# Performance work log

Hardware: AMD Instinct MI355X
Metric: run time of the kernel (lower is better)

Reference implementation:

```python
import jax, jax.numpy as jnp
import numpy as np

B, T, C, H, E, K = 4, 2048, 512, 2048, 8, 2


def setup_inputs() -> dict:
    key = jax.random.key(0)
    ks = jax.random.split(key, 7)
    s_r = 1.0 / np.sqrt(C)
    s_h = 1.0 / np.sqrt(H)
    return {
        "x": jax.random.normal(ks[0], (B, T, C), dtype=jnp.float32),
        "Wr": jax.random.uniform(ks[1], (C, E), jnp.float32, -s_r, s_r),
        "br": jax.random.uniform(ks[2], (E,), jnp.float32, -s_r, s_r),
        "W1": jax.random.uniform(ks[3], (E, C, H), jnp.float32, -s_r, s_r),
        "b1": jax.random.uniform(ks[4], (E, H), jnp.float32, -s_r, s_r),
        "W2": jax.random.uniform(ks[5], (E, H, C), jnp.float32, -s_h, s_h),
        "b2": jax.random.uniform(ks[6], (E, C), jnp.float32, -s_h, s_h),
    }


def reference(x, Wr, br, W1, b1, W2, b2):
    # Router logits [B,T,E]
    logits = jnp.einsum("btc,ce->bte", x, Wr) + br
    topk_vals, topk_idx = jax.lax.top_k(logits, K)  # [B,T,K]
    scores = jax.nn.softmax(topk_vals, axis=-1)  # softmax over the K selected
    # Combine weights per expert: gate[b,t,e] = sum_k scores[b,t,k]*(idx==e)
    onehot = jax.nn.one_hot(topk_idx, E, dtype=x.dtype)  # [B,T,K,E]
    gate = jnp.einsum("btk,btke->bte", scores, onehot)  # [B,T,E]
    # Dense-masked expert MLPs (tokens not routed to e have gate==0)
    h = jax.nn.relu(jnp.einsum("btc,ech->bteh", x, W1) + b1)  # [B,T,E,H]
    y = jnp.einsum("bteh,ehc->btec", h, W2) + b2  # [B,T,E,C]
    out = jnp.einsum("btec,bte->btc", y, gate)  # weighted combine
    return logits, topk_idx, out
```

## Files before the change

### kernel.cpp

```cpp
#include <hip/hip_runtime.h>
#include <hip/hip_bf16.h>

#define NTOK 8192
#define NASN 16384
#define C_ 512
#define H_ 2048
#define E_ 8
#define RBC 2048

typedef __bf16 bf16x8 __attribute__((ext_vector_type(8)));
typedef float f32x4 __attribute__((ext_vector_type(4)));

#define WS_COUNTS 0
#define WS_OFFS   65536
#define WS_T1S    65792
#define WS_INFO   66048
#define WS_TOKL   (WS_INFO + NTOK*16)
#define WS_SLOTS  (WS_TOKL + NASN*4)
#define WS_XBF    (WS_SLOTS + NTOK*8)
#define WS_W1B    (WS_XBF + (size_t)NTOK*C_*2)
#define WS_W2B    (WS_W1B + (size_t)E_*H_*C_*2)
#define WS_HS     (WS_W2B + (size_t)E_*H_*C_*2)
#define WS_YS     WS_XBF

__device__ __forceinline__ unsigned int f2bf(float f) {
  __hip_bfloat16 h = __float2bfloat16(f);
  return (unsigned int)*(unsigned short*)&h;
}
__device__ __forceinline__ float bf2f(unsigned int u) {
  return __int_as_float((u & 0xffffu) << 16);
}

__device__ __forceinline__ void g2l16(const unsigned short* g, unsigned short* l) {
  __builtin_amdgcn_global_load_lds(
      (const __attribute__((address_space(1))) unsigned int*)g,
      (__attribute__((address_space(3))) unsigned int*)l, 16, 0, 0);
}

__device__ __forceinline__ void stage_decode(int L, int& brow, int& q) {
  int s = L >> 3, slot = L & 7;
  int v = slot ^ (s & 7);
  brow = 2*s + (v >> 2);
  q = v & 3;
}

__global__ __launch_bounds__(256) void k_fused(
    const float* __restrict__ x, const float* __restrict__ Wr,
    const float* __restrict__ br, float* __restrict__ out_logits,
    float* __restrict__ out_idx, int4* __restrict__ info,
    int* __restrict__ counts, unsigned short* __restrict__ Xbf,
    const float* __restrict__ W1, unsigned short* __restrict__ W1b,
    const float* __restrict__ W2, unsigned short* __restrict__ W2b)
{
  __shared__ float tileS[128][33];
  __shared__ int bc[8];
  int b = blockIdx.x;
  int tid = threadIdx.x;

  if (b < RBC) {
    if (tid < 8) bc[tid] = 0;
    __syncthreads();
    int t = b * 4 + (tid >> 6);
    int lane = tid & 63;
    const float4* xr = (const float4*)(x + (size_t)t * C_);
    float4 x0 = xr[lane*2], x1 = xr[lane*2+1];
    uint4 pk;
    pk.x = f2bf(x0.x) | (f2bf(x0.y) << 16);
    pk.y = f2bf(x0.z) | (f2bf(x0.w) << 16);
    pk.z = f2bf(x1.x) | (f2bf(x1.y) << 16);
    pk.w = f2bf(x1.z) | (f2bf(x1.w) << 16);
    *(uint4*)(Xbf + (size_t)t * C_ + lane*8) = pk;

    float xs[8] = {x0.x,x0.y,x0.z,x0.w,x1.x,x1.y,x1.z,x1.w};
    float acc[8] = {0,0,0,0,0,0,0,0};
    #pragma unroll
    for (int j = 0; j < 8; j++) {
      const float4* w = (const float4*)(Wr + (size_t)(lane*8+j) * E_);
      float4 w0 = w[0], w1 = w[1];
      float we[8] = {w0.x,w0.y,w0.z,w0.w,w1.x,w1.y,w1.z,w1.w};
      #pragma unroll
      for (int e = 0; e < 8; e++) acc[e] += xs[j] * we[e];
    }
    #pragma unroll
    for (int off = 1; off < 64; off <<= 1) {
      #pragma unroll
      for (int e = 0; e < 8; e++) acc[e] += __shfl_xor(acc[e], off, 64);
    }
    #pragma unroll
    for (int e = 0; e < 8; e++) acc[e] += br[e];
    if (lane == 0) {
      #pragma unroll
      for (int e = 0; e < 8; e++) out_logits[t*8 + e] = acc[e];
      int i0 = 0; float v0 = acc[0];
      #pragma unroll
      for (int e = 1; e < 8; e++) if (acc[e] > v0) { v0 = acc[e]; i0 = e; }
      int i1 = -1; float v1 = -1e30f;
      #pragma unroll
      for (int e = 0; e < 8; e++) if (e != i0 && acc[e] > v1) { v1 = acc[e]; i1 = e; }
      float d = expf(v1 - v0);
      float s1 = d / (1.0f + d);
      float s0 = 1.0f - s1;
      out_idx[t*2]     = (float)i0;
      out_idx[t*2 + 1] = (float)i1;
      info[t] = make_int4(i0, i1, __float_as_int(s0), __float_as_int(s1));
      atomicAdd(&bc[i0], 1);
      atomicAdd(&bc[i1], 1);
    }
    __syncthreads();
    if (tid < 8) counts[b*8 + tid] = bc[tid];
    return;
  }

  const float* in; unsigned short* outp; int R, S, bx, by, bz;
  if (b < 2*RBC) {
    int bb = b - RBC;
    in = W1; outp = W1b; R = C_; S = H_;
    bx = bb & 63; by = (bb >> 6) & 3; bz = bb >> 8;
  } else {
    int bb = b - 2*RBC;
    in = W2; outp = W2b; R = H_; S = C_;
    bx = bb & 15; by = (bb >> 4) & 15; bz = bb >> 8;
  }
  size_t zo = (size_t)bz * R * S;
  in += zo; outp += zo;
  int r0 = by * 128, s0 = bx * 32;
  #pragma unroll
  for (int i = 0; i < 16; i++) {
    int lin = i*256 + tid;
    int rr = lin >> 5, ss = lin & 31;
    tileS[rr][ss] = in[(size_t)(r0 + rr) * S + s0 + ss];
  }
  __syncthreads();
  #pragma unroll
  for (int i = 0; i < 4; i++) {
    int lin = i*256 + tid;
    int ss = lin >> 5, rq = lin & 31;
    ushort4 v;
    v.x = (unsigned short)f2bf(tileS[rq*4+0][ss]);
    v.y = (unsigned short)f2bf(tileS[rq*4+1][ss]);
    v.z = (unsigned short)f2bf(tileS[rq*4+2][ss]);
    v.w = (unsigned short)f2bf(tileS[rq*4+3][ss]);
    *(ushort4*)(outp + (size_t)(s0 + ss) * R + r0 + rq*4) = v;
  }
}

__global__ __launch_bounds__(64) void k_prefscatter(
    const int* __restrict__ counts, const int4* __restrict__ info,
    int* __restrict__ tokl, int2* __restrict__ slots2,
    int* __restrict__ offs, int* __restrict__ t1s)
{
  __shared__ int full_s[8][8];
  __shared__ int part_s[8][8];
  __shared__ int tot_s[8];
  __shared__ int off_s[9];
  __shared__ int cur[8];
  int c = blockIdx.x, t = threadIdx.x;
  int e = t & 7, g = t >> 3;
  int lim = c * 16;
  int full = 0, part = 0;
  for (int i = 0; i < 256; i++) {
    int rb = g*256 + i;
    int v = counts[rb*8 + e];
    full += v;
    if (rb < lim) part += v;
  }
  full_s[e][g] = full; part_s[e][g] = part;
  __syncthreads();
  if (t < 8) {
    int s = 0;
    #pragma unroll
    for (int gg = 0; gg < 8; gg++) s += full_s[t][gg];
    tot_s[t] = s;
  }
  __syncthreads();
  if (t == 0) {
    int o = 0;
    off_s[0] = 0;
    for (int ee = 0; ee < 8; ee++) { o += tot_s[ee]; off_s[ee+1] = o; }
    if (c == 0) {
      offs[0] = 0; t1s[0] = 0;
      int tt = 0;
      for (int ee = 0; ee < 8; ee++) {
        offs[ee+1] = off_s[ee+1];
        tt += (tot_s[ee] + 127) >> 7;
        t1s[ee+1] = tt;
      }
    }
  }
  __syncthreads();
  if (t < 8) {
    int mg = c >> 4;
    int bse = off_s[t];
    #pragma unroll
    for (int gg = 0; gg < 8; gg++) if (gg < mg) bse += full_s[t][gg];
    bse += part_s[t][mg];
    cur[t] = bse;
  }
  __syncthreads();
  int tok = c*64 + t;
  int4 nfo = info[tok];
  int r0 = atomicAdd(&cur[nfo.x], 1);
  int r1 = atomicAdd(&cur[nfo.y], 1);
  tokl[r0] = tok;
  tokl[r1] = tok;
  slots2[tok] = make_int2(r0, r1);
}

#define KLOOP(KI)                                                              \
  {                                                                            \
    int cOff = 0, sOff = 2*8192;                                               \
    for (int ki = 0; ki < (KI); ki++) {                                        \
      if (ki + 1 < (KI))                                                       \
        asm volatile("s_waitcnt vmcnt(2)" ::: "memory");                       \
      else                                                                     \
        asm volatile("s_waitcnt vmcnt(0)" ::: "memory");                       \
      asm volatile("s_barrier" ::: "memory");                                  \
      if (ki + 2 < (KI)) {                                                     \
        int off_ = (ki + 2) * 32;                                              \
        unsigned short* nb_ = AB + sOff;                                       \
        g2l16(ga + off_, nb_ + lao);                                           \
        g2l16(gb + off_, nb_ + lbo);                                           \
      }                                                                        \
      const unsigned short* Ap_ = AB + cOff;                                   \
      const unsigned short* Bp_ = Ap_ + 4096;                                  \
      bf16x8 af0 = *(const bf16x8*)&Ap_[wm*32 + 0*512 + rbase];                \
      bf16x8 af1 = *(const bf16x8*)&Ap_[wm*32 + 1*512 + rbase];                \
      bf16x8 bf0 = *(const bf16x8*)&Bp_[wn*32 + 0*512 + rbase];                \
      bf16x8 bf1 = *(const bf16x8*)&Bp_[wn*32 + 1*512 + rbase];                \
      __builtin_amdgcn_s_setprio(1);                                           \
      acc[0][0] = __builtin_amdgcn_mfma_f32_16x16x32_bf16(af0, bf0, acc[0][0], 0, 0, 0); \
      acc[0][1] = __builtin_amdgcn_mfma_f32_16x16x32_bf16(af0, bf1, acc[0][1], 0, 0, 0); \
      acc[1][0] = __builtin_amdgcn_mfma_f32_16x16x32_bf16(af1, bf0, acc[1][0], 0, 0, 0); \
      acc[1][1] = __builtin_amdgcn_mfma_f32_16x16x32_bf16(af1, bf1, acc[1][1], 0, 0, 0); \
      __builtin_amdgcn_s_setprio(0);                                           \
      bf16x8 af2 = *(const bf16x8*)&Ap_[wm*32 + 2*512 + rbase];                \
      bf16x8 af3 = *(const bf16x8*)&Ap_[wm*32 + 3*512 + rbase];                \
      __builtin_amdgcn_s_setprio(1);                                           \
      acc[2][0] = __builtin_amdgcn_mfma_f32_16x16x32_bf16(af2, bf0, acc[2][0], 0, 0, 0); \
      acc[2][1] = __builtin_amdgcn_mfma_f32_16x16x32_bf16(af2, bf1, acc[2][1], 0, 0, 0); \
      acc[3][0] = __builtin_amdgcn_mfma_f32_16x16x32_bf16(af3, bf0, acc[3][0], 0, 0, 0); \
      acc[3][1] = __builtin_amdgcn_mfma_f32_16x16x32_bf16(af3, bf1, acc[3][1], 0, 0, 0); \
      __builtin_amdgcn_s_setprio(0);                                           \
      asm volatile("s_waitcnt lgkmcnt(0)" ::: "memory");                       \
      cOff += 8192; if (cOff == 3*8192) cOff = 0;                              \
      sOff += 8192; if (sOff == 3*8192) sOff = 0;                              \
    }                                                                          \
  }

__global__ __launch_bounds__(512) void k_gemm1(
    const unsigned short* __restrict__ Xbf, const int* __restrict__ tokl,
    const unsigned short* __restrict__ W1b,
    const float* __restrict__ b1, unsigned short* __restrict__ Hs,
    const int* __restrict__ offs, const int* __restrict__ t1s)
{
  __shared__ __align__(16) unsigned short AB[3*8192];
  int b = blockIdx.x;
  int mo = b >> 7, rr = b & 127;
  int n0 = (rr >> 3) * 128;
  int mt = mo*8 + (rr & 7);
  if (mt >= t1s[8]) return;
  int e = 0;
  #pragma unroll
  for (int i = 0; i < 7; i++) if (mt >= t1s[e+1]) e++;
  int row0 = offs[e] + (mt - t1s[e]) * 128;
  int rowEnd = offs[e+1];
  int tid = threadIdx.x, lane = tid & 63, w = tid >> 6;
  int wm = (w >> 2) * 64, wn = (w & 3) * 32;
  int quad = lane >> 4, l16 = lane & 15;
  const f32x4 zero = {0.f, 0.f, 0.f, 0.f};
  f32x4 acc[4][2];
  #pragma unroll
  for (int i = 0; i < 4; i++)
    #pragma unroll
    for (int j = 0; j < 2; j++) acc[i][j] = zero;
  const unsigned short* Bsrc = W1b + ((size_t)e * H_ + n0) * C_;

  const unsigned short* ga; const unsigned short* gb;
  int lao, lbo;
  {
    int L = w*64 + lane;
    int brow, q; stage_decode(L, brow, q);
    int gr = row0 + brow; gr = gr < NASN-1 ? gr : NASN-1;
    int trow = tokl[gr];
    ga = Xbf + (size_t)trow * C_ + q*8;
    gb = Bsrc + (size_t)brow * C_ + q*8;
    lao = w*512;
    lbo = 4096 + w*512;
  }
  int rbase = (l16>>1)*64 + ((((l16&1)<<2) + quad) ^ (l16>>1))*8;
  const int KI = C_ / 32;

  g2l16(ga, AB + lao);            g2l16(gb, AB + lbo);
  g2l16(ga + 32, AB + 8192 + lao); g2l16(gb + 32, AB + 8192 + lbo);

  KLOOP(KI);

  unsigned short* Lt = AB + w*2048;
  #pragma unroll
  for (int j = 0; j < 2; j++) {
    int n = n0 + wn + j*16 + l16;
    float bias = b1[e * H_ + n];
    #pragma unroll
    for (int i = 0; i < 4; i++)
      #pragma unroll
      for (int r = 0; r < 4; r++) {
        float v = acc[i][j][r] + bias;
        Lt[(i*16 + quad*4 + r)*32 + j*16 + l16] = (unsigned short)f2bf(v > 0.f ? v : 0.f);
      }
  }
  #pragma unroll
  for (int it = 0; it < 4; it++) {
    int rloc = it*16 + (lane >> 2);
    int m = row0 + wm + rloc;
    uint4 vv = *(uint4*)&Lt[rloc*32 + (lane & 3)*8];
    if (m < rowEnd)
      *(uint4*)(Hs + (size_t)m * H_ + n0 + wn + (lane & 3)*8) = vv;
  }
}

__global__ __launch_bounds__(512) void k_gemm2(
    const unsigned short* __restrict__ Hs, const unsigned short* __restrict__ W2b,
    const float* __restrict__ b2, unsigned short* __restrict__ Ys,
    const int* __restrict__ offs, const int* __restrict__ t1s)
{
  __shared__ __align__(16) unsigned short AB[3*8192];
  int b = blockIdx.x;
  int mo = b >> 5, rr = b & 31;
  int n0 = (rr >> 3) * 128;
  int mt = mo*8 + (rr & 7);
  if (mt >= t1s[8]) return;
  int e = 0;
  #pragma unroll
  for (int i = 0; i < 7; i++) if (mt >= t1s[e+1]) e++;
  int row0 = offs[e] + (mt - t1s[e]) * 128;
  int rowEnd = offs[e+1];
  int tid = threadIdx.x, lane = tid & 63, w = tid >> 6;
  int wm = (w >> 2) * 64, wn = (w & 3) * 32;
  int quad = lane >> 4, l16 = lane & 15;
  const f32x4 zero = {0.f, 0.f, 0.f, 0.f};
  f32x4 acc[4][2];
  #pragma unroll
  for (int i = 0; i < 4; i++)
    #pragma unroll
    for (int j = 0; j < 2; j++) acc[i][j] = zero;
  const unsigned short* Bsrc = W2b + ((size_t)e * C_ + n0) * H_;

  const unsigned short* ga; const unsigned short* gb;
  int lao, lbo;
  {
    int L = w*64 + lane;
    int brow, q; stage_decode(L, brow, q);
    int gr = row0 + brow; gr = gr < NASN-1 ? gr : NASN-1;
    ga = Hs + (size_t)gr * H_ + q*8;
    gb = Bsrc + (size_t)brow * H_ + q*8;
    lao = w*512;
    lbo = 4096 + w*512;
  }
  int rbase = (l16>>1)*64 + ((((l16&1)<<2) + quad) ^ (l16>>1))*8;
  const int KI = H_ / 32;

  g2l16(ga, AB + lao);            g2l16(gb, AB + lbo);
  g2l16(ga + 32, AB + 8192 + lao); g2l16(gb + 32, AB + 8192 + lbo);

  KLOOP(KI);

  unsigned short* Lt = AB + w*2048;
  #pragma unroll
  for (int j = 0; j < 2; j++) {
    int n = n0 + wn + j*16 + l16;
    float bias = b2[e * C_ + n];
    #pragma unroll
    for (int i = 0; i < 4; i++)
      #pragma unroll
      for (int r = 0; r < 4; r++)
        Lt[(i*16 + quad*4 + r)*32 + j*16 + l16] =
            (unsigned short)f2bf(acc[i][j][r] + bias);
  }
  #pragma unroll
  for (int it = 0; it < 4; it++) {
    int rloc = it*16 + (lane >> 2);
    int m = row0 + wm + rloc;
    uint4 vv = *(uint4*)&Lt[rloc*32 + (lane & 3)*8];
    if (m < rowEnd)
      *(uint4*)(Ys + (size_t)m * C_ + n0 + wn + (lane & 3)*8) = vv;
  }
}

__global__ __launch_bounds__(256) void k_combine(
    const unsigned short* __restrict__ Ys, const int4* __restrict__ info,
    const int2* __restrict__ slots2, float* __restrict__ outp)
{
  int t = blockIdx.x * 4 + (threadIdx.x >> 6);
  int lane = threadIdx.x & 63;
  int4 nfo = info[t];
  int2 ss = slots2[t];
  float g0 = __int_as_float(nfo.z), g1 = __int_as_float(nfo.w);
  uint4 a = *(const uint4*)(Ys + (size_t)ss.x * C_ + lane*8);
  uint4 bb = *(const uint4*)(Ys + (size_t)ss.y * C_ + lane*8);
  unsigned int au[4] = {a.x, a.y, a.z, a.w};
  unsigned int bu[4] = {bb.x, bb.y, bb.z, bb.w};
  float vals[8];
  #pragma unroll
  for (int q = 0; q < 4; q++) {
    vals[q*2]   = g0*bf2f(au[q])       + g1*bf2f(bu[q]);
    vals[q*2+1] = g0*bf2f(au[q] >> 16) + g1*bf2f(bu[q] >> 16);
  }
  float4 o0, o1;
  o0.x = vals[0]; o0.y = vals[1]; o0.z = vals[2]; o0.w = vals[3];
  o1.x = vals[4]; o1.y = vals[5]; o1.z = vals[6]; o1.w = vals[7];
  float4* o = (float4*)(outp + (size_t)t * C_ + lane*8);
  o[0] = o0;
  o[1] = o1;
}

extern "C" void kernel_launch(void* const* d_in, const int* in_sizes, int n_in,
                              void* d_out, int out_size, void* d_ws, size_t ws_size,
                              hipStream_t stream)
{
  const float* x  = (const float*)d_in[0];
  const float* Wr = (const float*)d_in[1];
  const float* br = (const float*)d_in[2];
  const float* W1 = (const float*)d_in[3];
  const float* b1 = (const float*)d_in[4];
  const float* W2 = (const float*)d_in[5];
  const float* b2 = (const float*)d_in[6];
  float* out = (float*)d_out;
  char* ws = (char*)d_ws;

  int*  counts = (int*)(ws + WS_COUNTS);
  int*  offs   = (int*)(ws + WS_OFFS);
  int*  t1s    = (int*)(ws + WS_T1S);
  int4* info   = (int4*)(ws + WS_INFO);
  int*  tokl   = (int*)(ws + WS_TOKL);
  int2* slots2 = (int2*)(ws + WS_SLOTS);
  unsigned short* Xbf = (unsigned short*)(ws + WS_XBF);
  unsigned short* W1b = (unsigned short*)(ws + WS_W1B);
  unsigned short* W2b = (unsigned short*)(ws + WS_W2B);
  unsigned short* Hs  = (unsigned short*)(ws + WS_HS);
  unsigned short* Ys  = (unsigned short*)(ws + WS_YS);

  k_fused<<<3*RBC, 256, 0, stream>>>(x, Wr, br, out, out + 65536, info,
                                     counts, Xbf, W1, W1b, W2, W2b);
  k_prefscatter<<<128, 64, 0, stream>>>(counts, info, tokl, slots2, offs, t1s);
  k_gemm1<<<17*128, 512, 0, stream>>>(Xbf, tokl, W1b, b1, Hs, offs, t1s);
  k_gemm2<<<17*32, 512, 0, stream>>>(Hs, W2b, b2, Ys, offs, t1s);
  k_combine<<<NTOK/4, 256, 0, stream>>>(Ys, info, slots2, out + 81920);
}
```

Measured before the change: 266.8 us.

## Use 2 warps per 128x128 GEMM tile with 64x128 per-warp subtiles

Both expert GEMM kernels now launch 128 threads (2 waves) per 128x128 output tile instead of 512 (8 waves). Each wave computes a 64x128 subtile with 32 MFMA accumulators, reusing each A fragment across 8 B fragments. Each thread issues 4x more global-to-LDS copies, and the vmcnt wait is raised to match. This cuts LDS fragment reads per MFMA, at the cost of far more accumulator registers, lower occupancy and fewer waves to hide latency.

```diff
diff --git a/kernel.cpp b/kernel.cpp
--- a/kernel.cpp
+++ b/kernel.cpp
@@ -211,35 +211,35 @@
     int cOff = 0, sOff = 2*8192;                                               \
     for (int ki = 0; ki < (KI); ki++) {                                        \
       if (ki + 1 < (KI))                                                       \
-        asm volatile("s_waitcnt vmcnt(2)" ::: "memory");                       \
+        asm volatile("s_waitcnt vmcnt(8)" ::: "memory");                       \
       else                                                                     \
         asm volatile("s_waitcnt vmcnt(0)" ::: "memory");                       \
       asm volatile("s_barrier" ::: "memory");                                  \
       if (ki + 2 < (KI)) {                                                     \
         int off_ = (ki + 2) * 32;                                              \
         unsigned short* nb_ = AB + sOff;                                       \
-        g2l16(ga + off_, nb_ + lao);                                           \
-        g2l16(gb + off_, nb_ + lbo);                                           \
+        _Pragma("unroll")                                                      \
+        for (int j = 0; j < 4; j++) {                                          \
+          g2l16(ga[j] + off_, nb_ + lao[j]);                                   \
+          g2l16(gb[j] + off_, nb_ + lbo[j]);                                   \
+        }                                                                      \
       }                                                                        \
       const unsigned short* Ap_ = AB + cOff;                                   \
       const unsigned short* Bp_ = Ap_ + 4096;                                  \
-      bf16x8 af0 = *(const bf16x8*)&Ap_[wm*32 + 0*512 + rbase];                \
-      bf16x8 af1 = *(const bf16x8*)&Ap_[wm*32 + 1*512 + rbase];                \
-      bf16x8 bf0 = *(const bf16x8*)&Bp_[wn*32 + 0*512 + rbase];                \
-      bf16x8 bf1 = *(const bf16x8*)&Bp_[wn*32 + 1*512 + rbase];                \
+      bf16x8 af_[4], bf_[8];                                                   \
+      _Pragma("unroll")                                                        \
+      for (int i = 0; i < 4; i++)                                              \
+        af_[i] = *(const bf16x8*)&Ap_[wmul + i*512 + rbase];                   \
+      _Pragma("unroll")                                                        \
+      for (int j = 0; j < 8; j++)                                              \
+        bf_[j] = *(const bf16x8*)&Bp_[j*512 + rbase];                          \
       __builtin_amdgcn_s_setprio(1);                                           \
-      acc[0][0] = __builtin_amdgcn_mfma_f32_16x16x32_bf16(af0, bf0, acc[0][0], 0, 0, 0); \
-      acc[0][1] = __builtin_amdgcn_mfma_f32_16x16x32_bf16(af0, bf1, acc[0][1], 0, 0, 0); \
-      acc[1][0] = __builtin_amdgcn_mfma_f32_16x16x32_bf16(af1, bf0, acc[1][0], 0, 0, 0); \
-      acc[1][1] = __builtin_amdgcn_mfma_f32_16x16x32_bf16(af1, bf1, acc[1][1], 0, 0, 0); \
-      __builtin_amdgcn_s_setprio(0);                                           \
-      bf16x8 af2 = *(const bf16x8*)&Ap_[wm*32 + 2*512 + rbase];                \
-      bf16x8 af3 = *(const bf16x8*)&Ap_[wm*32 + 3*512 + rbase];                \
-      __builtin_amdgcn_s_setprio(1);                                           \
-      acc[2][0] = __builtin_amdgcn_mfma_f32_16x16x32_bf16(af2, bf0, acc[2][0], 0, 0, 0); \
-      acc[2][1] = __builtin_amdgcn_mfma_f32_16x16x32_bf16(af2, bf1, acc[2][1], 0, 0, 0); \
-      acc[3][0] = __builtin_amdgcn_mfma_f32_16x16x32_bf16(af3, bf0, acc[3][0], 0, 0, 0); \
-      acc[3][1] = __builtin_amdgcn_mfma_f32_16x16x32_bf16(af3, bf1, acc[3][1], 0, 0, 0); \
+      _Pragma("unroll")                                                        \
+      for (int i = 0; i < 4; i++)                                              \
+        _Pragma("unroll")                                                      \
+        for (int j = 0; j < 8; j++)                                            \
+          acc[i][j] = __builtin_amdgcn_mfma_f32_16x16x32_bf16(                 \
+              af_[i], bf_[j], acc[i][j], 0, 0, 0);                             \
       __builtin_amdgcn_s_setprio(0);                                           \
       asm volatile("s_waitcnt lgkmcnt(0)" ::: "memory");                       \
       cOff += 8192; if (cOff == 3*8192) cOff = 0;                              \
@@ -247,7 +247,7 @@
     }                                                                          \
   }
 
-__global__ __launch_bounds__(512) void k_gemm1(
+__global__ __launch_bounds__(128) void k_gemm1(
     const unsigned short* __restrict__ Xbf, const int* __restrict__ tokl,
     const unsigned short* __restrict__ W1b,
     const float* __restrict__ b1, unsigned short* __restrict__ Hs,
@@ -265,60 +265,63 @@
   int row0 = offs[e] + (mt - t1s[e]) * 128;
   int rowEnd = offs[e+1];
   int tid = threadIdx.x, lane = tid & 63, w = tid >> 6;
-  int wm = (w >> 2) * 64, wn = (w & 3) * 32;
+  int wmul = w * 2048;
   int quad = lane >> 4, l16 = lane & 15;
   const f32x4 zero = {0.f, 0.f, 0.f, 0.f};
-  f32x4 acc[4][2];
+  f32x4 acc[4][8];
   #pragma unroll
   for (int i = 0; i < 4; i++)
     #pragma unroll
-    for (int j = 0; j < 2; j++) acc[i][j] = zero;
+    for (int j = 0; j < 8; j++) acc[i][j] = zero;
   const unsigned short* Bsrc = W1b + ((size_t)e * H_ + n0) * C_;
 
-  const unsigned short* ga; const unsigned short* gb;
-  int lao, lbo;
-  {
-    int L = w*64 + lane;
+  const unsigned short* ga[4]; const unsigned short* gb[4];
+  int lao[4], lbo[4];
+  #pragma unroll
+  for (int j = 0; j < 4; j++) {
+    int L = (w*4 + j)*64 + lane;
     int brow, q; stage_decode(L, brow, q);
     int gr = row0 + brow; gr = gr < NASN-1 ? gr : NASN-1;
     int trow = tokl[gr];
-    ga = Xbf + (size_t)trow * C_ + q*8;
-    gb = Bsrc + (size_t)brow * C_ + q*8;
-    lao = w*512;
-    lbo = 4096 + w*512;
+    ga[j] = Xbf + (size_t)trow * C_ + q*8;
+    gb[j] = Bsrc + (size_t)brow * C_ + q*8;
+    lao[j] = (w*4 + j)*512;
+    lbo[j] = 4096 + (w*4 + j)*512;
   }
   int rbase = (l16>>1)*64 + ((((l16&1)<<2) + quad) ^ (l16>>1))*8;
   const int KI = C_ / 32;
 
-  g2l16(ga, AB + lao);            g2l16(gb, AB + lbo);
-  g2l16(ga + 32, AB + 8192 + lao); g2l16(gb + 32, AB + 8192 + lbo);
+  #pragma unroll
+  for (int j = 0; j < 4; j++) { g2l16(ga[j], AB + lao[j]); g2l16(gb[j], AB + lbo[j]); }
+  #pragma unroll
+  for (int j = 0; j < 4; j++) { g2l16(ga[j] + 32, AB + 8192 + lao[j]); g2l16(gb[j] + 32, AB + 8192 + lbo[j]); }
 
   KLOOP(KI);
 
-  unsigned short* Lt = AB + w*2048;
-  #pragma unroll
-  for (int j = 0; j < 2; j++) {
-    int n = n0 + wn + j*16 + l16;
+  unsigned short* Lt = AB + w*8192;
+  #pragma unroll
+  for (int j = 0; j < 8; j++) {
+    int n = n0 + j*16 + l16;
     float bias = b1[e * H_ + n];
     #pragma unroll
     for (int i = 0; i < 4; i++)
       #pragma unroll
       for (int r = 0; r < 4; r++) {
         float v = acc[i][j][r] + bias;
-        Lt[(i*16 + quad*4 + r)*32 + j*16 + l16] = (unsigned short)f2bf(v > 0.f ? v : 0.f);
+        Lt[(i*16 + quad*4 + r)*128 + j*16 + l16] = (unsigned short)f2bf(v > 0.f ? v : 0.f);
       }
   }
   #pragma unroll
-  for (int it = 0; it < 4; it++) {
-    int rloc = it*16 + (lane >> 2);
-    int m = row0 + wm + rloc;
-    uint4 vv = *(uint4*)&Lt[rloc*32 + (lane & 3)*8];
+  for (int it = 0; it < 16; it++) {
+    int rloc = it*4 + (lane >> 4);
+    int m = row0 + w*64 + rloc;
+    uint4 vv = *(uint4*)&Lt[rloc*128 + (lane & 15)*8];
     if (m < rowEnd)
-      *(uint4*)(Hs + (size_t)m * H_ + n0 + wn + (lane & 3)*8) = vv;
-  }
-}
-
-__global__ __launch_bounds__(512) void k_gemm2(
+      *(uint4*)(Hs + (size_t)m * H_ + n0 + (lane & 15)*8) = vv;
+  }
+}
+
+__global__ __launch_bounds__(128) void k_gemm2(
     const unsigned short* __restrict__ Hs, const unsigned short* __restrict__ W2b,
     const float* __restrict__ b2, unsigned short* __restrict__ Ys,
     const int* __restrict__ offs, const int* __restrict__ t1s)
@@ -335,54 +338,57 @@
   int row0 = offs[e] + (mt - t1s[e]) * 128;
   int rowEnd = offs[e+1];
   int tid = threadIdx.x, lane = tid & 63, w = tid >> 6;
-  int wm = (w >> 2) * 64, wn = (w & 3) * 32;
+  int wmul = w * 2048;
   int quad = lane >> 4, l16 = lane & 15;
   const f32x4 zero = {0.f, 0.f, 0.f, 0.f};
-  f32x4 acc[4][2];
+  f32x4 acc[4][8];
   #pragma unroll
   for (int i = 0; i < 4; i++)
     #pragma unroll
-    for (int j = 0; j < 2; j++) acc[i][j] = zero;
+    for (int j = 0; j < 8; j++) acc[i][j] = zero;
   const unsigned short* Bsrc = W2b + ((size_t)e * C_ + n0) * H_;
 
-  const unsigned short* ga; const unsigned short* gb;
-  int lao, lbo;
-  {
-    int L = w*64 + lane;
+  const unsigned short* ga[4]; const unsigned short* gb[4];
+  int lao[4], lbo[4];
+  #pragma unroll
+  for (int j = 0; j < 4; j++) {
+    int L = (w*4 + j)*64 + lane;
     int brow, q; stage_decode(L, brow, q);
     int gr = row0 + brow; gr = gr < NASN-1 ? gr : NASN-1;
-    ga = Hs + (size_t)gr * H_ + q*8;
-    gb = Bsrc + (size_t)brow * H_ + q*8;
-    lao = w*512;
-    lbo = 4096 + w*512;
+    ga[j] = Hs + (size_t)gr * H_ + q*8;
+    gb[j] = Bsrc + (size_t)brow * H_ + q*8;
+    lao[j] = (w*4 + j)*512;
+    lbo[j] = 4096 + (w*4 + j)*512;
   }
   int rbase = (l16>>1)*64 + ((((l16&1)<<2) + quad) ^ (l16>>1))*8;
   const int KI = H_ / 32;
 
-  g2l16(ga, AB + lao);            g2l16(gb, AB + lbo);
-  g2l16(ga + 32, AB + 8192 + lao); g2l16(gb + 32, AB + 8192 + lbo);
+  #pragma unroll
+  for (int j = 0; j < 4; j++) { g2l16(ga[j], AB + lao[j]); g2l16(gb[j], AB + lbo[j]); }
+  #pragma unroll
+  for (int j = 0; j < 4; j++) { g2l16(ga[j] + 32, AB + 8192 + lao[j]); g2l16(gb[j] + 32, AB + 8192 + lbo[j]); }
 
   KLOOP(KI);
 
-  unsigned short* Lt = AB + w*2048;
-  #pragma unroll
-  for (int j = 0; j < 2; j++) {
-    int n = n0 + wn + j*16 + l16;
+  unsigned short* Lt = AB + w*8192;
+  #pragma unroll
+  for (int j = 0; j < 8; j++) {
+    int n = n0 + j*16 + l16;
     float bias = b2[e * C_ + n];
     #pragma unroll
     for (int i = 0; i < 4; i++)
       #pragma unroll
       for (int r = 0; r < 4; r++)
-        Lt[(i*16 + quad*4 + r)*32 + j*16 + l16] =
+        Lt[(i*16 + quad*4 + r)*128 + j*16 + l16] =
             (unsigned short)f2bf(acc[i][j][r] + bias);
   }
   #pragma unroll
-  for (int it = 0; it < 4; it++) {
-    int rloc = it*16 + (lane >> 2);
-    int m = row0 + wm + rloc;
-    uint4 vv = *(uint4*)&Lt[rloc*32 + (lane & 3)*8];
+  for (int it = 0; it < 16; it++) {
+    int rloc = it*4 + (lane >> 4);
+    int m = row0 + w*64 + rloc;
+    uint4 vv = *(uint4*)&Lt[rloc*128 + (lane & 15)*8];
     if (m < rowEnd)
-      *(uint4*)(Ys + (size_t)m * C_ + n0 + wn + (lane & 3)*8) = vv;
+      *(uint4*)(Ys + (size_t)m * C_ + n0 + (lane & 15)*8) = vv;
   }
 }
 
@@ -442,7 +448,7 @@
   k_fused<<<3*RBC, 256, 0, stream>>>(x, Wr, br, out, out + 65536, info,
                                      counts, Xbf, W1, W1b, W2, W2b);
   k_prefscatter<<<128, 64, 0, stream>>>(counts, info, tokl, slots2, offs, t1s);
-  k_gemm1<<<17*128, 512, 0, stream>>>(Xbf, tokl, W1b, b1, Hs, offs, t1s);
-  k_gemm2<<<17*32, 512, 0, stream>>>(Hs, W2b, b2, Ys, offs, t1s);
+  k_gemm1<<<17*128, 128, 0, stream>>>(Xbf, tokl, W1b, b1, Hs, offs, t1s);
+  k_gemm2<<<17*32, 128, 0, stream>>>(Hs, W2b, b2, Ys, offs, t1s);
   k_combine<<<NTOK/4, 256, 0, stream>>>(Ys, info, slots2, out + 81920);
 }
```

After: 324.9 us. +21.8%, slower.

## Convert expert GEMMs to persistent kernels with atomic tile queues

Applied to the files above, without the earlier changes.

The grouped GEMM kernels become persistent: a fixed grid of workgroups pulls tile indices from a global atomic counter that the prefix/scatter kernel resets, instead of launching a worst-case grid where most blocks exit early. The goal is to cut launch and early-exit overhead and balance tiles across CUs. The cost is an atomic and an extra barrier per tile. Tile order also changes so that the N-tiles of one M-tile are consecutive, which alters weight and activation cache reuse.

```diff
diff --git a/kernel.cpp b/kernel.cpp
--- a/kernel.cpp
+++ b/kernel.cpp
@@ -14,6 +14,7 @@
 #define WS_COUNTS 0
 #define WS_OFFS   65536
 #define WS_T1S    65792
+#define WS_QC     65856
 #define WS_INFO   66048
 #define WS_TOKL   (WS_INFO + NTOK*16)
 #define WS_SLOTS  (WS_TOKL + NASN*4)
@@ -147,7 +148,7 @@
 __global__ __launch_bounds__(64) void k_prefscatter(
     const int* __restrict__ counts, const int4* __restrict__ info,
     int* __restrict__ tokl, int2* __restrict__ slots2,
-    int* __restrict__ offs, int* __restrict__ t1s)
+    int* __restrict__ offs, int* __restrict__ t1s, int* __restrict__ qc)
 {
   __shared__ int full_s[8][8];
   __shared__ int part_s[8][8];
@@ -179,6 +180,7 @@
     for (int ee = 0; ee < 8; ee++) { o += tot_s[ee]; off_s[ee+1] = o; }
     if (c == 0) {
       offs[0] = 0; t1s[0] = 0;
+      qc[0] = 0; qc[1] = 0;
       int tt = 0;
       for (int ee = 0; ee < 8; ee++) {
         offs[ee+1] = off_s[ee+1];
@@ -251,138 +253,154 @@
     const unsigned short* __restrict__ Xbf, const int* __restrict__ tokl,
     const unsigned short* __restrict__ W1b,
     const float* __restrict__ b1, unsigned short* __restrict__ Hs,
-    const int* __restrict__ offs, const int* __restrict__ t1s)
+    const int* __restrict__ offs, const int* __restrict__ t1s,
+    int* __restrict__ qc)
 {
   __shared__ __align__(16) unsigned short AB[3*8192];
-  int b = blockIdx.x;
-  int mo = b >> 7, rr = b & 127;
-  int n0 = (rr >> 3) * 128;
-  int mt = mo*8 + (rr & 7);
-  if (mt >= t1s[8]) return;
-  int e = 0;
-  #pragma unroll
-  for (int i = 0; i < 7; i++) if (mt >= t1s[e+1]) e++;
-  int row0 = offs[e] + (mt - t1s[e]) * 128;
-  int rowEnd = offs[e+1];
+  __shared__ int tsh;
   int tid = threadIdx.x, lane = tid & 63, w = tid >> 6;
   int wm = (w >> 2) * 64, wn = (w & 3) * 32;
   int quad = lane >> 4, l16 = lane & 15;
-  const f32x4 zero = {0.f, 0.f, 0.f, 0.f};
-  f32x4 acc[4][2];
-  #pragma unroll
-  for (int i = 0; i < 4; i++)
-    #pragma unroll
-    for (int j = 0; j < 2; j++) acc[i][j] = zero;
-  const unsigned short* Bsrc = W1b + ((size_t)e * H_ + n0) * C_;
-
-  const unsigned short* ga; const unsigned short* gb;
-  int lao, lbo;
-  {
-    int L = w*64 + lane;
-    int brow, q; stage_decode(L, brow, q);
-    int gr = row0 + brow; gr = gr < NASN-1 ? gr : NASN-1;
-    int trow = tokl[gr];
-    ga = Xbf + (size_t)trow * C_ + q*8;
-    gb = Bsrc + (size_t)brow * C_ + q*8;
-    lao = w*512;
-    lbo = 4096 + w*512;
-  }
   int rbase = (l16>>1)*64 + ((((l16&1)<<2) + quad) ^ (l16>>1))*8;
   const int KI = C_ / 32;
-
-  g2l16(ga, AB + lao);            g2l16(gb, AB + lbo);
-  g2l16(ga + 32, AB + 8192 + lao); g2l16(gb + 32, AB + 8192 + lbo);
-
-  KLOOP(KI);
-
-  unsigned short* Lt = AB + w*2048;
-  #pragma unroll
-  for (int j = 0; j < 2; j++) {
-    int n = n0 + wn + j*16 + l16;
-    float bias = b1[e * H_ + n];
+  int nTiles = t1s[8] * 16;
+  const f32x4 zero = {0.f, 0.f, 0.f, 0.f};
+
+  for (;;) {
+    if (tid == 0) tsh = atomicAdd(qc, 1);
+    __syncthreads();
+    int ti = tsh;
+    if (ti >= nTiles) break;
+    int n0 = (ti & 15) * 128;
+    int mt = ti >> 4;
+    int e = 0;
+    #pragma unroll
+    for (int i = 0; i < 7; i++) if (mt >= t1s[i+1]) e++;
+    int row0 = offs[e] + (mt - t1s[e]) * 128;
+    int rowEnd = offs[e+1];
+    f32x4 acc[4][2];
     #pragma unroll
     for (int i = 0; i < 4; i++)
       #pragma unroll
-      for (int r = 0; r < 4; r++) {
-        float v = acc[i][j][r] + bias;
-        Lt[(i*16 + quad*4 + r)*32 + j*16 + l16] = (unsigned short)f2bf(v > 0.f ? v : 0.f);
-      }
-  }
-  #pragma unroll
-  for (int it = 0; it < 4; it++) {
-    int rloc = it*16 + (lane >> 2);
-    int m = row0 + wm + rloc;
-    uint4 vv = *(uint4*)&Lt[rloc*32 + (lane & 3)*8];
-    if (m < rowEnd)
-      *(uint4*)(Hs + (size_t)m * H_ + n0 + wn + (lane & 3)*8) = vv;
+      for (int j = 0; j < 2; j++) acc[i][j] = zero;
+    const unsigned short* Bsrc = W1b + ((size_t)e * H_ + n0) * C_;
+
+    const unsigned short* ga; const unsigned short* gb;
+    int lao, lbo;
+    {
+      int L = w*64 + lane;
+      int brow, q; stage_decode(L, brow, q);
+      int gr = row0 + brow; gr = gr < NASN-1 ? gr : NASN-1;
+      int trow = tokl[gr];
+      ga = Xbf + (size_t)trow * C_ + q*8;
+      gb = Bsrc + (size_t)brow * C_ + q*8;
+      lao = w*512;
+      lbo = 4096 + w*512;
+    }
+
+    g2l16(ga, AB + lao);             g2l16(gb, AB + lbo);
+    g2l16(ga + 32, AB + 8192 + lao); g2l16(gb + 32, AB + 8192 + lbo);
+
+    KLOOP(KI);
+    __syncthreads();
+
+    unsigned short* Lt = AB + w*2048;
+    #pragma unroll
+    for (int j = 0; j < 2; j++) {
+      int n = n0 + wn + j*16 + l16;
+      float bias = b1[e * H_ + n];
+      #pragma unroll
+      for (int i = 0; i < 4; i++)
+        #pragma unroll
+        for (int r = 0; r < 4; r++) {
+          float v = acc[i][j][r] + bias;
+          Lt[(i*16 + quad*4 + r)*32 + j*16 + l16] = (unsigned short)f2bf(v > 0.f ? v : 0.f);
+        }
+    }
+    #pragma unroll
+    for (int it = 0; it < 4; it++) {
+      int rloc = it*16 + (lane >> 2);
+      int m = row0 + wm + rloc;
+      uint4 vv = *(uint4*)&Lt[rloc*32 + (lane & 3)*8];
+      if (m < rowEnd)
+        *(uint4*)(Hs + (size_t)m * H_ + n0 + wn + (lane & 3)*8) = vv;
+    }
   }
 }
 
 __global__ __launch_bounds__(512) void k_gemm2(
     const unsigned short* __restrict__ Hs, const unsigned short* __restrict__ W2b,
     const float* __restrict__ b2, unsigned short* __restrict__ Ys,
-    const int* __restrict__ offs, const int* __restrict__ t1s)
+    const int* __restrict__ offs, const int* __restrict__ t1s,
+    int* __restrict__ qc)
 {
   __shared__ __align__(16) unsigned short AB[3*8192];
-  int b = blockIdx.x;
-  int mo = b >> 5, rr = b & 31;
-  int n0 = (rr >> 3) * 128;
-  int mt = mo*8 + (rr & 7);
-  if (mt >= t1s[8]) return;
-  int e = 0;
-  #pragma unroll
-  for (int i = 0; i < 7; i++) if (mt >= t1s[e+1]) e++;
-  int row0 = offs[e] + (mt - t1s[e]) * 128;
-  int rowEnd = offs[e+1];
+  __shared__ int tsh;
   int tid = threadIdx.x, lane = tid & 63, w = tid >> 6;
   int wm = (w >> 2) * 64, wn = (w & 3) * 32;
   int quad = lane >> 4, l16 = lane & 15;
-  const f32x4 zero = {0.f, 0.f, 0.f, 0.f};
-  f32x4 acc[4][2];
-  #pragma unroll
-  for (int i = 0; i < 4; i++)
-    #pragma unroll
-    for (int j = 0; j < 2; j++) acc[i][j] = zero;
-  const unsigned short* Bsrc = W2b + ((size_t)e * C_ + n0) * H_;
-
-  const unsigned short* ga; const unsigned short* gb;
-  int lao, lbo;
-  {
-    int L = w*64 + lane;
-    int brow, q; stage_decode(L, brow, q);
-    int gr = row0 + brow; gr = gr < NASN-1 ? gr : NASN-1;
-    ga = Hs + (size_t)gr * H_ + q*8;
-    gb = Bsrc + (size_t)brow * H_ + q*8;
-    lao = w*512;
-    lbo = 4096 + w*512;
-  }
   int rbase = (l16>>1)*64 + ((((l16&1)<<2) + quad) ^ (l16>>1))*8;
   const int KI = H_ / 32;
-
-  g2l16(ga, AB + lao);            g2l16(gb, AB + lbo);
-  g2l16(ga + 32, AB + 8192 + lao); g2l16(gb + 32, AB + 8192 + lbo);
-
-  KLOOP(KI);
-
-  unsigned short* Lt = AB + w*2048;
-  #pragma unroll
-  for (int j = 0; j < 2; j++) {
-    int n = n0 + wn + j*16 + l16;
-    float bias = b2[e * C_ + n];
+  int nTiles = t1s[8] * 4;
+  const f32x4 zero = {0.f, 0.f, 0.f, 0.f};
+
+  for (;;) {
+    if (tid == 0) tsh = atomicAdd(qc, 1);
+    __syncthreads();
+    int ti = tsh;
+    if (ti >= nTiles) break;
+    int n0 = (ti & 3) * 128;
+    int mt = ti >> 2;
+    int e = 0;
+    #pragma unroll
+    for (int i = 0; i < 7; i++) if (mt >= t1s[i+1]) e++;
+    int row0 = offs[e] + (mt - t1s[e]) * 128;
+    int rowEnd = offs[e+1];
+    f32x4 acc[4][2];
     #pragma unroll
     for (int i = 0; i < 4; i++)
       #pragma unroll
-      for (int r = 0; r < 4; r++)
-        Lt[(i*16 + quad*4 + r)*32 + j*16 + l16] =
-            (unsigned short)f2bf(acc[i][j][r] + bias);
-  }
-  #pragma unroll
-  for (int it = 0; it < 4; it++) {
-    int rloc = it*16 + (lane >> 2);
-    int m = row0 + wm + rloc;
-    uint4 vv = *(uint4*)&Lt[rloc*32 + (lane & 3)*8];
-    if (m < rowEnd)
-      *(uint4*)(Ys + (size_t)m * C_ + n0 + wn + (lane & 3)*8) = vv;
+      for (int j = 0; j < 2; j++) acc[i][j] = zero;
+    const unsigned short* Bsrc = W2b + ((size_t)e * C_ + n0) * H_;
+
+    const unsigned short* ga; const unsigned short* gb;
+    int lao, lbo;
+    {
+      int L = w*64 + lane;
+      int brow, q; stage_decode(L, brow, q);
+      int gr = row0 + brow; gr = gr < NASN-1 ? gr : NASN-1;
+      ga = Hs + (size_t)gr * H_ + q*8;
+      gb = Bsrc + (size_t)brow * H_ + q*8;
+      lao = w*512;
+      lbo = 4096 + w*512;
+    }
+
+    g2l16(ga, AB + lao);             g2l16(gb, AB + lbo);
+    g2l16(ga + 32, AB + 8192 + lao); g2l16(gb + 32, AB + 8192 + lbo);
+
+    KLOOP(KI);
+    __syncthreads();
+
+    unsigned short* Lt = AB + w*2048;
+    #pragma unroll
+    for (int j = 0; j < 2; j++) {
+      int n = n0 + wn + j*16 + l16;
+      float bias = b2[e * C_ + n];
+      #pragma unroll
+      for (int i = 0; i < 4; i++)
+        #pragma unroll
+        for (int r = 0; r < 4; r++)
+          Lt[(i*16 + quad*4 + r)*32 + j*16 + l16] =
+              (unsigned short)f2bf(acc[i][j][r] + bias);
+    }
+    #pragma unroll
+    for (int it = 0; it < 4; it++) {
+      int rloc = it*16 + (lane >> 2);
+      int m = row0 + wm + rloc;
+      uint4 vv = *(uint4*)&Lt[rloc*32 + (lane & 3)*8];
+      if (m < rowEnd)
+        *(uint4*)(Ys + (size_t)m * C_ + n0 + wn + (lane & 3)*8) = vv;
+    }
   }
 }
 
@@ -430,6 +448,7 @@
   int*  counts = (int*)(ws + WS_COUNTS);
   int*  offs   = (int*)(ws + WS_OFFS);
   int*  t1s    = (int*)(ws + WS_T1S);
+  int*  qc     = (int*)(ws + WS_QC);
   int4* info   = (int4*)(ws + WS_INFO);
   int*  tokl   = (int*)(ws + WS_TOKL);
   int2* slots2 = (int2*)(ws + WS_SLOTS);
@@ -441,8 +460,8 @@
 
   k_fused<<<3*RBC, 256, 0, stream>>>(x, Wr, br, out, out + 65536, info,
                                      counts, Xbf, W1, W1b, W2, W2b);
-  k_prefscatter<<<128, 64, 0, stream>>>(counts, info, tokl, slots2, offs, t1s);
-  k_gemm1<<<17*128, 512, 0, stream>>>(Xbf, tokl, W1b, b1, Hs, offs, t1s);
-  k_gemm2<<<17*32, 512, 0, stream>>>(Hs, W2b, b2, Ys, offs, t1s);
+  k_prefscatter<<<128, 64, 0, stream>>>(counts, info, tokl, slots2, offs, t1s, qc);
+  k_gemm1<<<768, 512, 0, stream>>>(Xbf, tokl, W1b, b1, Hs, offs, t1s, qc);
+  k_gemm2<<<512, 512, 0, stream>>>(Hs, W2b, b2, Ys, offs, t1s, qc + 1);
   k_combine<<<NTOK/4, 256, 0, stream>>>(Ys, info, slots2, out + 81920);
 }
```

New measurement: 299.2 us. 12.1% more time.
